# Performance work log

Measured on AMD Instinct MI355X. Metric: run time of the kernel, lower is better.

## Reference

```python
import jax, jax.numpy as jnp
import numpy as np

D_MODEL = 768
N_HEADS = 12
D_K = D_MODEL // N_HEADS
WINDOW = 256
NEG_INF = -1e30


def setup_inputs() -> dict:
    key = jax.random.key(0)
    ks = jax.random.split(key, 9)
    s = 0.02
    x = jax.random.normal(ks[0], (2, 2048, D_MODEL), dtype=jnp.float32)
    Wq = jax.random.normal(ks[1], (D_MODEL, D_MODEL), dtype=jnp.float32) * s
    bq = jnp.zeros((D_MODEL,), dtype=jnp.float32)
    Wk = jax.random.normal(ks[2], (D_MODEL, D_MODEL), dtype=jnp.float32) * s
    bk = jnp.zeros((D_MODEL,), dtype=jnp.float32)
    Wv = jax.random.normal(ks[3], (D_MODEL, D_MODEL), dtype=jnp.float32) * s
    bv = jnp.zeros((D_MODEL,), dtype=jnp.float32)
    Wo = jax.random.normal(ks[4], (D_MODEL, D_MODEL), dtype=jnp.float32) * s
    bo = jnp.zeros((D_MODEL,), dtype=jnp.float32)
    return {"x": x, "Wq": Wq, "bq": bq, "Wk": Wk, "bk": bk,
            "Wv": Wv, "bv": bv, "Wo": Wo, "bo": bo}


def _window_mask(seq_len: int) -> jnp.ndarray:
    # Faithful to _apply_sliding_window_attention: scores are reshaped into
    # (nw, ws, nw, ws) windows and a causal tril is applied broadcast over BOTH
    # window indices => position (q, k) allowed iff (q % ws) >= (k % ws).
    # (seq_len here is a multiple of WINDOW, so pad/slice is a no-op.)
    if seq_len <= WINDOW:
        q = jnp.arange(seq_len)
        return q[:, None] >= jnp.arange(seq_len)[None, :]
    qmod = jnp.arange(seq_len) % WINDOW
    return qmod[:, None] >= qmod[None, :]


def reference(x, Wq, bq, Wk, bk, Wv, bv, Wo, bo):
    B, S, _ = x.shape
    # torch nn.Linear: y = x @ W.T + b
    q = (x @ Wq.T + bq).reshape(B, S, N_HEADS, D_K).transpose(0, 2, 1, 3)
    k = (x @ Wk.T + bk).reshape(B, S, N_HEADS, D_K).transpose(0, 2, 1, 3)
    v = (x @ Wv.T + bv).reshape(B, S, N_HEADS, D_K).transpose(0, 2, 1, 3)
    scores = jnp.einsum('bhqd,bhkd->bhqk', q, k) / jnp.sqrt(jnp.float32(D_K))
    mask = _window_mask(S)  # [S, S] bool
    scores = jnp.where(mask[None, None, :, :], scores, NEG_INF)
    probs = jax.nn.softmax(scores, axis=-1)  # dropout p=0 (eval)
    out = jnp.einsum('bhqk,bhkd->bhqd', probs, v)
    out = out.transpose(0, 2, 1, 3).reshape(B, S, D_MODEL)
    return out @ Wo.T + bo
```

## Files before the change

### kernel.cpp

```cpp
#include <hip/hip_runtime.h>

typedef unsigned short u16;
typedef unsigned int u32;
typedef unsigned long long u64;
typedef __attribute__((ext_vector_type(8))) short bfrag;
typedef __attribute__((ext_vector_type(4))) float f32x4;
typedef __attribute__((ext_vector_type(16))) float f32x16;
typedef __attribute__((ext_vector_type(4))) u32 u32x4;

#define QSCALE 0.18033688f

__device__ __forceinline__ u16 f2bf(float f) {
    unsigned u = __float_as_uint(f);
    u += 0x7FFFu + ((u >> 16) & 1u);
    return (u16)(u >> 16);
}

__device__ __forceinline__ u32 cvt_pk_bf16(float lo, float hi) {
    u32 r;
    asm("v_cvt_pk_bf16_f32 %0, %1, %2" : "=v"(r) : "v"(lo), "v"(hi));
    return r;
}

__device__ __forceinline__ float fexp2(float x) {
    float r;
    asm("v_exp_f32 %0, %1" : "=v"(r) : "v"(x));
    return r;
}

__device__ __forceinline__ void glds16(const void* g, void* l) {
    __builtin_amdgcn_global_load_lds((__attribute__((address_space(1))) void*)g,
                                     (__attribute__((address_space(3))) void*)l,
                                     16, 0, 0);
}

__device__ __forceinline__ f32x16 mfma32(bfrag a, bfrag b, f32x16 c) {
    return __builtin_amdgcn_mfma_f32_32x32x16_bf16(a, b, c, 0, 0, 0);
}

#define WAIT_VM4()  asm volatile("s_waitcnt vmcnt(4)" ::: "memory")
#define WAIT_VM3()  asm volatile("s_waitcnt vmcnt(3)" ::: "memory")
#define WAIT_VM2()  asm volatile("s_waitcnt vmcnt(2)" ::: "memory")
#define WAIT_VM0()  asm volatile("s_waitcnt vmcnt(0)" ::: "memory")
#define BAR()       __builtin_amdgcn_s_barrier()
#define SCHED_FENCE() __builtin_amdgcn_sched_barrier(0)

__global__ __launch_bounds__(256) void convert_all(
    const float* __restrict__ x, const float* __restrict__ wq,
    const float* __restrict__ wk, const float* __restrict__ wv,
    const float* __restrict__ wo,
    u16* __restrict__ xb, u16* __restrict__ wqb, u16* __restrict__ wkb,
    u16* __restrict__ wvb, u16* __restrict__ wob) {
    const int XV = (2 * 2048 * 768) / 4;
    const int WV = (768 * 768) / 4;
    int i = blockIdx.x * 256 + threadIdx.x;
    if (i >= XV + 4 * WV) return;
    const float4* src; u16* dst; int off;
    if (i < XV) { src = (const float4*)x; dst = xb; off = i; }
    else {
        int j = i - XV; int z = j / WV; off = j - z * WV;
        src = (const float4*)(z == 0 ? wq : z == 1 ? wk : z == 2 ? wv : wo);
        dst = (z == 0 ? wqb : z == 1 ? wkb : z == 2 ? wvb : wob);
    }
    float4 v = src[off];
    u64 pk = (u64)f2bf(v.x)
        | ((u64)f2bf(v.y) << 16)
        | ((u64)f2bf(v.z) << 32)
        | ((u64)f2bf(v.w) << 48);
    *(u64*)(dst + off * 4) = pk;
}

__device__ __forceinline__ void gemm_core(
    const u16* __restrict__ A, const u16* __restrict__ Bw, int m0,
    u16* a_lds, u16* b_lds, f32x4 acc[4][4]) {
    const int t = threadIdx.x;
    const int w = t >> 6, lane = t & 63, ln = lane & 15, lh = lane >> 4;
    const int wr = w >> 1, wc = w & 1;

    const int row0 = t >> 2;
    const int u0 = (t & 3) ^ ((row0 >> 1) & 3);
    const int row1 = row0 + 64;
    const int u1 = (t & 3) ^ ((row1 >> 1) & 3);
    const u16* ga0 = A + (m0 + row0) * 768 + u0 * 8;
    const u16* ga1 = A + (m0 + row1) * 768 + u1 * 8;
    const u16* gb0 = Bw + row0 * 768 + u0 * 8;
    const u16* gb1 = Bw + row1 * 768 + u1 * 8;
    u16* la = a_lds + w * 512;
    u16* lb = b_lds + w * 512;

    auto STAGE = [&](int k0, int bi) {
        glds16(ga0 + k0, la + bi * 4096);
        glds16(ga1 + k0, la + bi * 4096 + 2048);
        glds16(gb0 + k0, lb + bi * 4096);
        glds16(gb1 + k0, lb + bi * 4096 + 2048);
    };

    STAGE(0, 0);
    int cur = 0;
    for (int k0 = 0; k0 < 768; k0 += 32) {
        if (k0 + 32 < 768) {
            STAGE(k0 + 32, cur ^ 1);
            WAIT_VM4();
        } else {
            WAIT_VM0();
        }
        BAR();
        SCHED_FENCE();
        const u16* ab = a_lds + cur * 4096;
        const u16* bb = b_lds + cur * 4096;
        bfrag aF[4], bF[4];
#pragma unroll
        for (int i = 0; i < 4; i++) {
            int ra = wr * 64 + i * 16 + ln;
            aF[i] = *(const bfrag*)(ab + ra * 32 + ((lh ^ ((ra >> 1) & 3)) * 8));
            int rb = wc * 64 + i * 16 + ln;
            bF[i] = *(const bfrag*)(bb + rb * 32 + ((lh ^ ((rb >> 1) & 3)) * 8));
        }
#pragma unroll
        for (int i = 0; i < 4; i++)
#pragma unroll
            for (int j = 0; j < 4; j++)
                acc[i][j] = __builtin_amdgcn_mfma_f32_16x16x32_bf16(
                    aF[i], bF[j], acc[i][j], 0, 0, 0);
        SCHED_FENCE();
        BAR();
        cur ^= 1;
    }
}

__global__ __launch_bounds__(256) void gemm_qkv(
    const u16* __restrict__ xb,
    const u16* __restrict__ wqb, const u16* __restrict__ wkb, const u16* __restrict__ wvb,
    const float* __restrict__ bq, const float* __restrict__ bk, const float* __restrict__ bv,
    u16* __restrict__ q_ws, u16* __restrict__ k_ws, u16* __restrict__ vt_ws) {
    __shared__ __align__(16) u16 smem[16384];
    u16* a_lds = smem;
    u16* b_lds = smem + 8192;
    const int m0 = blockIdx.x * 128;
    const int z = blockIdx.y / 6, nb = blockIdx.y % 6;
    const u16* Bw = (z == 0 ? wqb : z == 1 ? wkb : wvb) + nb * 128 * 768;
    const float* bias = (z == 0 ? bq : z == 1 ? bk : bv);

    f32x4 acc[4][4] = {};
    gemm_core(xb, Bw, m0, a_lds, b_lds, acc);

    const int t = threadIdx.x, w = t >> 6, lane = t & 63, ln = lane & 15, lh = lane >> 4;
    const int wr = w >> 1, wc = w & 1;
    if (z == 2) {
        __syncthreads();
        char* T = (char*)smem;
#pragma unroll
        for (int j = 0; j < 4; j++) {
            int nt = wc * 64 + j * 16 + ln;
            float bb = bias[nb * 128 + nt];
#pragma unroll
            for (int i = 0; i < 4; i++) {
                int m0t = wr * 64 + i * 16 + lh * 4;
                u64 pk = (u64)f2bf(acc[i][j][0] + bb)
                    | ((u64)f2bf(acc[i][j][1] + bb) << 16)
                    | ((u64)f2bf(acc[i][j][2] + bb) << 32)
                    | ((u64)f2bf(acc[i][j][3] + bb) << 48);
                int off = nt * 256 + ((m0t * 2) ^ ((nt & 15) << 4));
                *(u64*)(T + off) = pk;
            }
        }
        __syncthreads();
        const int b = m0 >> 11, s0 = m0 & 2047;
#pragma unroll
        for (int c = 0; c < 8; c++) {
            int g = c * 256 + t;
            int nt = g >> 4, mc = (g & 15) * 8;
            int off = nt * 256 + ((mc * 2) ^ ((nt & 15) << 4));
            u32x4 v = *(const u32x4*)(T + off);
            int nl = nb * 128 + nt;
            int h = nl >> 6, d = nl & 63;
            *(u32x4*)(vt_ws + ((size_t)((b * 12 + h) * 64 + d)) * 2048 + s0 + mc) = v;
        }
    } else {
        u16* dst = (z == 0 ? q_ws : k_ws);
        const float sc = (z == 0) ? QSCALE : 1.0f;
#pragma unroll
        for (int j = 0; j < 4; j++) {
            int nl = nb * 128 + wc * 64 + j * 16 + ln;
            int h = nl >> 6, d = nl & 63;
            float bb = bias[nl];
#pragma unroll
            for (int i = 0; i < 4; i++)
#pragma unroll
                for (int r = 0; r < 4; r++) {
                    int m = m0 + wr * 64 + i * 16 + lh * 4 + r;
                    int b = m >> 11, s = m & 2047;
                    dst[((size_t)((b * 12 + h) * 2048 + s)) * 64 + d] = f2bf((acc[i][j][r] + bb) * sc);
                }
        }
    }
}

__device__ __forceinline__ void gemm_core64(
    const u16* __restrict__ A, const u16* __restrict__ Bw, int m0,
    u16* a_lds, u16* b_lds, f32x4 acc[2][4]) {
    const int t = threadIdx.x;
    const int w = t >> 6, lane = t & 63, ln = lane & 15, lh = lane >> 4;
    const int wr = w >> 1, wc = w & 1;

    const int rowA = t >> 2;
    const int uA = (t & 3) ^ ((rowA >> 1) & 3);
    const int rowB1 = rowA + 64;
    const int uB1 = (t & 3) ^ ((rowB1 >> 1) & 3);
    const u16* ga  = A + (m0 + rowA) * 768 + uA * 8;
    const u16* gb0 = Bw + rowA * 768 + uA * 8;
    const u16* gb1 = Bw + rowB1 * 768 + uB1 * 8;
    u16* la = a_lds + w * 512;
    u16* lb = b_lds + w * 512;

    auto STAGE = [&](int k0, int bi) {
        glds16(ga + k0, la + bi * 2048);
        glds16(gb0 + k0, lb + bi * 4096);
        glds16(gb1 + k0, lb + bi * 4096 + 2048);
    };

    STAGE(0, 0);
    int cur = 0, nxt = 1;
    for (int k0 = 0; k0 < 768; k0 += 32) {
        if (k0 + 32 < 768) {
            STAGE(k0 + 32, nxt);
            WAIT_VM3();
        } else {
            WAIT_VM0();
        }
        BAR();
        SCHED_FENCE();
        const u16* ab = a_lds + cur * 2048;
        const u16* bb = b_lds + cur * 4096;
        bfrag aF[2], bF[4];
#pragma unroll
        for (int i = 0; i < 2; i++) {
            int ra = wr * 32 + i * 16 + ln;
            aF[i] = *(const bfrag*)(ab + ra * 32 + ((lh ^ ((ra >> 1) & 3)) * 8));
        }
#pragma unroll
        for (int j = 0; j < 4; j++) {
            int rb = wc * 64 + j * 16 + ln;
            bF[j] = *(const bfrag*)(bb + rb * 32 + ((lh ^ ((rb >> 1) & 3)) * 8));
        }
#pragma unroll
        for (int i = 0; i < 2; i++)
#pragma unroll
            for (int j = 0; j < 4; j++)
                acc[i][j] = __builtin_amdgcn_mfma_f32_16x16x32_bf16(
                    aF[i], bF[j], acc[i][j], 0, 0, 0);
        cur = nxt;
        nxt = (nxt == 2) ? 0 : nxt + 1;
    }
}

__global__ __launch_bounds__(256) void gemm_out64(
    const u16* __restrict__ ob, const u16* __restrict__ wob,
    const float* __restrict__ bo, float* __restrict__ out) {
    __shared__ __align__(16) u16 a_lds[3 * 64 * 32];
    __shared__ __align__(16) u16 b_lds[3 * 128 * 32];
    const int m0 = blockIdx.x * 64, n0 = blockIdx.y * 128;
    f32x4 acc[2][4] = {};
    gemm_core64(ob, wob + n0 * 768, m0, a_lds, b_lds, acc);
    const int t = threadIdx.x, w = t >> 6, lane = t & 63, ln = lane & 15, lh = lane >> 4;
    const int wr = w >> 1, wc = w & 1;
#pragma unroll
    for (int j = 0; j < 4; j++) {
        int n = n0 + wc * 64 + j * 16 + ln;
        float bb = bo[n];
#pragma unroll
        for (int i = 0; i < 2; i++)
#pragma unroll
            for (int r = 0; r < 4; r++) {
                int m = m0 + wr * 32 + i * 16 + lh * 4 + r;
                out[m * 768 + n] = acc[i][j][r] + bb;
            }
    }
}

__global__ __launch_bounds__(512) void attn14(
    const u16* __restrict__ q_ws, const u16* __restrict__ k_ws,
    const u16* __restrict__ vt_ws, u16* __restrict__ o_ws,
    u16* __restrict__ po_ws, float* __restrict__ l_ws) {
    __shared__ __align__(16) u16 k_lds[3][64 * 64];
    __shared__ __align__(16) u16 v_lds[3][64 * 64];

    const int t = threadIdx.x, w = t >> 6, l = t & 63, lq = l & 31, H = l >> 5;
    int id = blockIdx.x;
    int bh8 = id & 7, idq = id >> 3;
    int bhq = idq % 3, pg = idq / 3;
    int t7, piece;
    if (pg < 4)       { t7 = 7; piece = pg; }
    else if (pg < 8)  { t7 = 6; piece = pg - 4; }
    else if (pg < 11) { t7 = 5; piece = pg - 8; }
    else if (pg < 14) { t7 = 4; piece = pg - 11; }
    else if (pg < 16) { t7 = 3; piece = pg - 14; }
    else if (pg < 18) { t7 = 2; piece = pg - 16; }
    else if (pg == 18){ t7 = 1; piece = 0; }
    else              { t7 = 0; piece = 0; }
    const int np = (t7 + 2) >> 1;
    const int bh = bhq * 8 + bh8;
    const int ti = w;
    const int tile = t7 + 8 * ti;
    const int qw0 = tile * 32;

    const u16* Qb = q_ws + (size_t)bh * 2048 * 64;
    const u16* Kb = k_ws + (size_t)bh * 2048 * 64;
    const u16* Vt = vt_ws + (size_t)bh * 64 * 2048;

    const int lqp = (lq & 19) | ((lq & 4) << 1) | ((lq & 8) >> 1);
    const int ksw = lqp & 7;
    const int vsw = lq & 7;

    bfrag qF[4];
#pragma unroll
    for (int kd = 0; kd < 4; kd++)
        qF[kd] = *(const bfrag*)(Qb + (size_t)(qw0 + lq) * 64 + kd * 16 + H * 8);

    const f32x16 Z = {};
    f32x16 O0 = Z, O1 = Z;
    float lsum = 0.f;

    const int skey = t >> 3;
    const int su = (t & 7) ^ (skey & 7);

    auto STAGE = [&](int k0, int bi) {
        glds16(Kb + (size_t)(k0 + skey) * 64 + su * 8, (u16*)k_lds + bi * 4096 + w * 512);
        glds16(Vt + (size_t)skey * 2048 + k0 + su * 8, (u16*)v_lds + bi * 4096 + w * 512);
    };

    int gp0 = piece * 8;
    int win = gp0 / np, pb = gp0 - win * np;
    STAGE(win * 256 + pb * 64, 0);

    int cur = 0, nxt = 1;
    for (int j = 0; j < 8; ++j) {
        int winn = win, pbn = pb + 1;
        if (pbn == np) { pbn = 0; winn = win + 1; }
        if (j < 7) {
            STAGE(winn * 256 + pbn * 64, nxt);
            WAIT_VM2();
        } else {
            WAIT_VM0();
        }
        BAR();
        SCHED_FENCE();

        const int cb = 2 * pb;
        const bool c1 = (cb + 1) <= t7, d0 = (cb == t7), d1 = (cb + 1 == t7);
        const u16* kl = (const u16*)k_lds + cur * 4096;
        const u16* vl = (const u16*)v_lds + cur * 4096;

        f32x16 s0, s1;
        {
            bfrag kf = *(const bfrag*)(kl + lqp * 64 + ((H) ^ ksw) * 8);
            s0 = mfma32(kf, qF[0], Z);
#pragma unroll
            for (int kd = 1; kd < 4; kd++) {
                bfrag k2 = *(const bfrag*)(kl + lqp * 64 + ((kd * 2 + H) ^ ksw) * 8);
                s0 = mfma32(k2, qF[kd], s0);
            }
        }
        if (c1) {
            bfrag kf = *(const bfrag*)(kl + (32 + lqp) * 64 + ((H) ^ ksw) * 8);
            s1 = mfma32(kf, qF[0], Z);
#pragma unroll
            for (int kd = 1; kd < 4; kd++) {
                bfrag k2 = *(const bfrag*)(kl + (32 + lqp) * 64 + ((kd * 2 + H) ^ ksw) * 8);
                s1 = mfma32(k2, qF[kd], s1);
            }
        }

        float ps = 0.f;
        u32 pkA[8], pkB[8];
        if (d0) {
#pragma unroll
            for (int r2 = 0; r2 < 16; r2++) {
                int ka = (r2 & 3) + 4 * ((r2 >> 2) & 1) + 16 * (r2 >> 3) + 8 * H;
                if (ka > lq) s0[r2] = -1e30f;
            }
        }
#pragma unroll
        for (int i = 0; i < 8; i++) {
            float a = fexp2(s0[2 * i]), b2 = fexp2(s0[2 * i + 1]);
            ps += a + b2; pkA[i] = cvt_pk_bf16(a, b2);
        }
        if (c1) {
            if (d1) {
#pragma unroll
                for (int r2 = 0; r2 < 16; r2++) {
                    int ka = (r2 & 3) + 4 * ((r2 >> 2) & 1) + 16 * (r2 >> 3) + 8 * H;
                    if (ka > lq) s1[r2] = -1e30f;
                }
            }
#pragma unroll
            for (int i = 0; i < 8; i++) {
                float a = fexp2(s1[2 * i]), b2 = fexp2(s1[2 * i + 1]);
                ps += a + b2; pkB[i] = cvt_pk_bf16(a, b2);
            }
        }
        lsum += ps;

        {
            u32x4 a0 = {pkA[0], pkA[1], pkA[2], pkA[3]};
            u32x4 a1 = {pkA[4], pkA[5], pkA[6], pkA[7]};
            bfrag A0 = __builtin_bit_cast(bfrag, a0);
            bfrag A1 = __builtin_bit_cast(bfrag, a1);
            bfrag v00 = *(const bfrag*)(vl + lq * 64 + ((H) ^ vsw) * 8);
            bfrag v01 = *(const bfrag*)(vl + (32 + lq) * 64 + ((H) ^ vsw) * 8);
            bfrag v10 = *(const bfrag*)(vl + lq * 64 + ((2 + H) ^ vsw) * 8);
            bfrag v11 = *(const bfrag*)(vl + (32 + lq) * 64 + ((2 + H) ^ vsw) * 8);
            O0 = mfma32(A0, v00, O0);
            O1 = mfma32(A0, v01, O1);
            O0 = mfma32(A1, v10, O0);
            O1 = mfma32(A1, v11, O1);
        }
        if (c1) {
            u32x4 a0 = {pkB[0], pkB[1], pkB[2], pkB[3]};
            u32x4 a1 = {pkB[4], pkB[5], pkB[6], pkB[7]};
            bfrag A0 = __builtin_bit_cast(bfrag, a0);
            bfrag A1 = __builtin_bit_cast(bfrag, a1);
            bfrag v00 = *(const bfrag*)(vl + lq * 64 + ((4 + H) ^ vsw) * 8);
            bfrag v01 = *(const bfrag*)(vl + (32 + lq) * 64 + ((4 + H) ^ vsw) * 8);
            bfrag v10 = *(const bfrag*)(vl + lq * 64 + ((6 + H) ^ vsw) * 8);
            bfrag v11 = *(const bfrag*)(vl + (32 + lq) * 64 + ((6 + H) ^ vsw) * 8);
            O0 = mfma32(A0, v00, O0);
            O1 = mfma32(A0, v01, O1);
            O0 = mfma32(A1, v10, O0);
            O1 = mfma32(A1, v11, O1);
        }
        win = winn; pb = pbn;
        cur = nxt;
        nxt = (nxt == 2) ? 0 : nxt + 1;
    }

    float lsT = lsum + __shfl_xor(lsum, 32);
    if (np == 1) {
        float linv = 1.f / lsT;
        const int b = bh / 12, h = bh % 12;
#pragma unroll
        for (int r2 = 0; r2 < 16; r2++) {
            int row = (r2 & 3) + 8 * (r2 >> 2) + 4 * H;
            float fr = __shfl(linv, row);
            size_t base = ((size_t)(b * 2048 + qw0 + row)) * 768 + h * 64;
            o_ws[base + lq] = f2bf(O0[r2] * fr);
            o_ws[base + 32 + lq] = f2bf(O1[r2] * fr);
        }
    } else {
        const int cum8[8] = {0, 8, 16, 32, 48, 72, 96, 128};
        size_t pidx = (size_t)bh * 160 + cum8[t7] + ti * np + piece;
        u16* po = po_ws + pidx * 2048;
#pragma unroll
        for (int r2 = 0; r2 < 16; r2++) {
            int row = (r2 & 3) + 8 * (r2 >> 2) + 4 * H;
            po[row * 64 + lq] = f2bf(O0[r2]);
            po[row * 64 + 32 + lq] = f2bf(O1[r2]);
        }
        if (l < 32) l_ws[pidx * 32 + lq] = lsT;
    }
}

__global__ __launch_bounds__(256) void combine_o(
    const u16* __restrict__ po_ws, const float* __restrict__ l_ws,
    u16* __restrict__ o_ws) {
    int id = blockIdx.x;
    int bh8 = id & 7, idq = id >> 3;
    int bhq = idq % 3, r = idq / 3;
    int bh = bhq * 8 + bh8;
    int t7 = 2 + (r >> 3), ti = r & 7;
    int tile = t7 + 8 * ti;
    int np = (t7 + 2) >> 1;
    const int cum8[8] = {0, 8, 16, 32, 48, 72, 96, 128};
    size_t base = (size_t)bh * 160 + cum8[t7] + ti * np;
    int t = threadIdx.x;
    int q = t >> 3, d8 = (t & 7) * 8;
    float acc[8] = {0.f, 0.f, 0.f, 0.f, 0.f, 0.f, 0.f, 0.f};
    float lt = 0.f;
    for (int i = 0; i < np; i++) {
        lt += l_ws[(base + i) * 32 + q];
        bfrag v = *(const bfrag*)(po_ws + (base + i) * 2048 + q * 64 + d8);
#pragma unroll
        for (int e = 0; e < 8; e++)
            acc[e] += __uint_as_float(((u32)(u16)v[e]) << 16);
    }
    float inv = 1.f / lt;
    u32x4 pkv;
#pragma unroll
    for (int e = 0; e < 4; e++)
        pkv[e] = cvt_pk_bf16(acc[2 * e] * inv, acc[2 * e + 1] * inv);
    int b = bh / 12, h = bh % 12;
    size_t dst = ((size_t)(b * 2048 + tile * 32 + q)) * 768 + h * 64 + d8;
    *(u32x4*)(o_ws + dst) = pkv;
}

extern "C" void kernel_launch(void* const* d_in, const int* in_sizes, int n_in,
                              void* d_out, int out_size, void* d_ws, size_t ws_size,
                              hipStream_t stream) {
    const float* x  = (const float*)d_in[0];
    const float* Wq = (const float*)d_in[1];
    const float* bq = (const float*)d_in[2];
    const float* Wk = (const float*)d_in[3];
    const float* bk = (const float*)d_in[4];
    const float* Wv = (const float*)d_in[5];
    const float* bv = (const float*)d_in[6];
    const float* Wo = (const float*)d_in[7];
    const float* bo = (const float*)d_in[8];
    float* out = (float*)d_out;

    char* p = (char*)d_ws;
    u16*   q_ws  = (u16*)(p + 0);
    u16*   k_ws  = (u16*)(p + 6291456);
    u16*   vt_ws = (u16*)(p + 12582912);
    u16*   po_ws = (u16*)(p + 18874368);
    u16*   xb    = (u16*)(p + 18874368);
    u16*   wqb   = (u16*)(p + 25165824);
    u16*   wkb   = (u16*)(p + 26345472);
    u16*   wvb   = (u16*)(p + 27525120);
    float* l_ws  = (float*)(p + 34603008);
    u16*   wob   = (u16*)(p + 35094528);
    u16*   o_ws  = (u16*)(p + 36274176);

    convert_all<<<5376, 256, 0, stream>>>(x, Wq, Wk, Wv, Wo, xb, wqb, wkb, wvb, wob);
    gemm_qkv<<<dim3(32, 18), 256, 0, stream>>>(xb, wqb, wkb, wvb, bq, bk, bv, q_ws, k_ws, vt_ws);
    attn14<<<dim3(480), 512, 0, stream>>>(q_ws, k_ws, vt_ws, o_ws, po_ws, l_ws);
    combine_o<<<dim3(1152), 256, 0, stream>>>(po_ws, l_ws, o_ws);
    gemm_out64<<<dim3(64, 6), 256, 0, stream>>>(o_ws, wob, bo, out);
}
```

Baseline: 79.56 us.

## Fuse split-KV combine into attention via atomic last-block reduction

Removes the separate combine_o launch. Each attention block that writes partial outputs increments a per-(head, tile-group) atomic counter. The last arriving block then sums the bf16 partials and the row sums and writes the normalized output. Counters are zeroed inside the convert kernel. This saves one kernel launch and its pass over global memory, at the cost of threadfences, extra barriers, and serialized combine work on the tail blocks.

After: 224.1 us. 2.82x slower.

```diff
diff --git a/kernel.cpp b/kernel.cpp
--- a/kernel.cpp
+++ b/kernel.cpp
@@ -50,9 +50,10 @@
     const float* __restrict__ wk, const float* __restrict__ wv,
     const float* __restrict__ wo,
     u16* __restrict__ xb, u16* __restrict__ wqb, u16* __restrict__ wkb,
-    u16* __restrict__ wvb, u16* __restrict__ wob) {
+    u16* __restrict__ wvb, u16* __restrict__ wob, int* __restrict__ cnt) {
     const int XV = (2 * 2048 * 768) / 4;
     const int WV = (768 * 768) / 4;
+    if (blockIdx.x == 0 && threadIdx.x < 144) cnt[threadIdx.x] = 0;
     int i = blockIdx.x * 256 + threadIdx.x;
     if (i >= XV + 4 * WV) return;
     const float4* src; u16* dst; int off;
@@ -278,12 +279,13 @@
     }
 }
 
-__global__ __launch_bounds__(512) void attn14(
+__global__ __launch_bounds__(512) void attn15(
     const u16* __restrict__ q_ws, const u16* __restrict__ k_ws,
     const u16* __restrict__ vt_ws, u16* __restrict__ o_ws,
-    u16* __restrict__ po_ws, float* __restrict__ l_ws) {
+    u16* __restrict__ po_ws, float* __restrict__ l_ws, int* __restrict__ cnt) {
     __shared__ __align__(16) u16 k_lds[3][64 * 64];
     __shared__ __align__(16) u16 v_lds[3][64 * 64];
+    __shared__ int lastv;
 
     const int t = threadIdx.x, w = t >> 6, l = t & 63, lq = l & 31, H = l >> 5;
     int id = blockIdx.x;
@@ -434,10 +436,10 @@
         nxt = (nxt == 2) ? 0 : nxt + 1;
     }
 
+    const int b = bh / 12, h = bh % 12;
     float lsT = lsum + __shfl_xor(lsum, 32);
     if (np == 1) {
         float linv = 1.f / lsT;
-        const int b = bh / 12, h = bh % 12;
 #pragma unroll
         for (int r2 = 0; r2 < 16; r2++) {
             int row = (r2 & 3) + 8 * (r2 >> 2) + 4 * H;
@@ -457,40 +459,46 @@
             po[row * 64 + 32 + lq] = f2bf(O1[r2]);
         }
         if (l < 32) l_ws[pidx * 32 + lq] = lsT;
-    }
-}
-
-__global__ __launch_bounds__(256) void combine_o(
-    const u16* __restrict__ po_ws, const float* __restrict__ l_ws,
-    u16* __restrict__ o_ws) {
-    int id = blockIdx.x;
-    int bh8 = id & 7, idq = id >> 3;
-    int bhq = idq % 3, r = idq / 3;
-    int bh = bhq * 8 + bh8;
-    int t7 = 2 + (r >> 3), ti = r & 7;
-    int tile = t7 + 8 * ti;
-    int np = (t7 + 2) >> 1;
-    const int cum8[8] = {0, 8, 16, 32, 48, 72, 96, 128};
-    size_t base = (size_t)bh * 160 + cum8[t7] + ti * np;
-    int t = threadIdx.x;
-    int q = t >> 3, d8 = (t & 7) * 8;
-    float acc[8] = {0.f, 0.f, 0.f, 0.f, 0.f, 0.f, 0.f, 0.f};
-    float lt = 0.f;
-    for (int i = 0; i < np; i++) {
-        lt += l_ws[(base + i) * 32 + q];
-        bfrag v = *(const bfrag*)(po_ws + (base + i) * 2048 + q * 64 + d8);
-#pragma unroll
-        for (int e = 0; e < 8; e++)
-            acc[e] += __uint_as_float(((u32)(u16)v[e]) << 16);
-    }
-    float inv = 1.f / lt;
-    u32x4 pkv;
-#pragma unroll
-    for (int e = 0; e < 4; e++)
-        pkv[e] = cvt_pk_bf16(acc[2 * e] * inv, acc[2 * e + 1] * inv);
-    int b = bh / 12, h = bh % 12;
-    size_t dst = ((size_t)(b * 2048 + tile * 32 + q)) * 768 + h * 64 + d8;
-    *(u32x4*)(o_ws + dst) = pkv;
+
+        __threadfence();
+        __syncthreads();
+        if (t == 0)
+            lastv = (atomicAdd(cnt + bh * 6 + (t7 - 2), 1) == np - 1);
+        __syncthreads();
+        if (lastv) {
+            __threadfence();
+            size_t pbase = (size_t)bh * 160 + cum8[t7] + w * np;
+            int q = l & 31, dh = l >> 5;
+            float lt = 0.f;
+            for (int i = 0; i < np; i++) lt += l_ws[(pbase + i) * 32 + q];
+            float inv = 1.f / lt;
+            size_t obase = ((size_t)(b * 2048 + qw0 + q)) * 768 + h * 64 + dh * 32;
+#pragma unroll
+            for (int hf = 0; hf < 2; hf++) {
+                float acc[16];
+#pragma unroll
+                for (int e = 0; e < 16; e++) acc[e] = 0.f;
+                for (int i = 0; i < np; i++) {
+                    const u16* src = po_ws + (pbase + i) * 2048 + q * 64 + dh * 32 + hf * 16;
+                    bfrag v0 = *(const bfrag*)(src);
+                    bfrag v1 = *(const bfrag*)(src + 8);
+#pragma unroll
+                    for (int e = 0; e < 8; e++) {
+                        acc[e]     += __uint_as_float(((u32)(u16)v0[e]) << 16);
+                        acc[8 + e] += __uint_as_float(((u32)(u16)v1[e]) << 16);
+                    }
+                }
+                u32x4 pk0, pk1;
+#pragma unroll
+                for (int e = 0; e < 4; e++) {
+                    pk0[e] = cvt_pk_bf16(acc[2 * e] * inv, acc[2 * e + 1] * inv);
+                    pk1[e] = cvt_pk_bf16(acc[8 + 2 * e] * inv, acc[9 + 2 * e] * inv);
+                }
+                *(u32x4*)(o_ws + obase + hf * 16) = pk0;
+                *(u32x4*)(o_ws + obase + hf * 16 + 8) = pk1;
+            }
+        }
+    }
 }
 
 extern "C" void kernel_launch(void* const* d_in, const int* in_sizes, int n_in,
@@ -519,10 +527,10 @@
     float* l_ws  = (float*)(p + 34603008);
     u16*   wob   = (u16*)(p + 35094528);
     u16*   o_ws  = (u16*)(p + 36274176);
-
-    convert_all<<<5376, 256, 0, stream>>>(x, Wq, Wk, Wv, Wo, xb, wqb, wkb, wvb, wob);
+    int*   cnt   = (int*)(p + 42565632);
+
+    convert_all<<<5376, 256, 0, stream>>>(x, Wq, Wk, Wv, Wo, xb, wqb, wkb, wvb, wob, cnt);
     gemm_qkv<<<dim3(32, 18), 256, 0, stream>>>(xb, wqb, wkb, wvb, bq, bk, bv, q_ws, k_ws, vt_ws);
-    attn14<<<dim3(480), 512, 0, stream>>>(q_ws, k_ws, vt_ws, o_ws, po_ws, l_ws);
-    combine_o<<<dim3(1152), 256, 0, stream>>>(po_ws, l_ws, o_ws);
+    attn15<<<dim3(480), 512, 0, stream>>>(q_ws, k_ws, vt_ws, o_ws, po_ws, l_ws, cnt);
     gemm_out64<<<dim3(64, 6), 256, 0, stream>>>(o_ws, wob, bo, out);
 }
```
